# Kernel optimization log

Hardware: AMD Instinct MI355X
Metric: run time of the kernel (lower is better)

## Reference

```python
import jax, jax.numpy as jnp
import numpy as np

B, T, I, H, FC, O = 256, 4096, 63, 50, 64, 2


def setup_inputs() -> dict:
    key = jax.random.key(0)
    ks = jax.random.split(key, 9)
    s_ih = 1.0 / np.sqrt(H)
    inp = {
        "x": jax.random.normal(ks[0], (B, T, I), dtype=jnp.float32),
        # RNN params (PyTorch layout: W_ih [H, I], W_hh [H, H])
        "W_ih": jax.random.uniform(ks[1], (H, I), jnp.float32, -s_ih, s_ih),
        "b_ih": jax.random.uniform(ks[2], (H,), jnp.float32, -s_ih, s_ih),
        "W_hh": jax.random.uniform(ks[3], (H, H), jnp.float32, -s_ih, s_ih),
        "b_hh": jax.random.uniform(ks[4], (H,), jnp.float32, -s_ih, s_ih),
        # MLP head
        "W1": jax.random.uniform(ks[5], (FC, H), jnp.float32, -1.0 / np.sqrt(H), 1.0 / np.sqrt(H)),
        "b1": jax.random.uniform(ks[6], (FC,), jnp.float32, -1.0 / np.sqrt(H), 1.0 / np.sqrt(H)),
        "W2": jax.random.uniform(ks[7], (O, FC), jnp.float32, -1.0 / np.sqrt(FC), 1.0 / np.sqrt(FC)),
        "b2": jax.random.uniform(ks[8], (O,), jnp.float32, -1.0 / np.sqrt(FC), 1.0 / np.sqrt(FC)),
    }
    return inp


def reference(x, W_ih, b_ih, W_hh, b_hh, W1, b1, W2, b2):
    # Precompute input projection for all timesteps in one GEMM: [B, T, H]
    xz = jnp.einsum("bti,hi->bth", x, W_ih) + b_ih
    h0 = jnp.zeros((x.shape[0], W_hh.shape[0]), x.dtype)

    def step(h, xt):  # h: [B, H], xt: [B, H]
        h_new = jnp.tanh(xt + h @ W_hh.T + b_hh)
        return h_new, None

    # scan over time; only the final hidden state is needed (out[:, -1, :])
    hT, _ = jax.lax.scan(step, h0, jnp.swapaxes(xz, 0, 1))
    out = jax.nn.relu(hT @ W1.T + b1) @ W2.T + b2  # [B, O]
    probs = jax.nn.softmax(out, axis=1)
    return jnp.argmax(probs, axis=1).astype(jnp.float32)  # [B]
```

## Files before the change

### kernel.cpp

```cpp
#include <hip/hip_runtime.h>
#include <cstdint>
#include <cstddef>

#define BB 256
#define TT 4096
#define ID 63
#define HH 50
#define FCD 64

__device__ __forceinline__ float readlane_f(float v, int lane) {
    return __int_as_float(__builtin_amdgcn_readlane(__float_as_int(v), lane));
}

__device__ __forceinline__ float fast_tanh(float x) {
    float a = fabsf(x);
    float e = __builtin_amdgcn_exp2f(a * -2.88539008177792681472f);
    float r = (1.0f - e) * __builtin_amdgcn_rcpf(1.0f + e);
    return copysignf(r, x);
}

__global__ __launch_bounds__(64) void proj_kernel(
    const float* __restrict__ x, const float* __restrict__ W_ih,
    const float* __restrict__ b_ih, const float* __restrict__ b_hh,
    float* __restrict__ z)
{
    __shared__ float xs[64 * ID];
    const int lane = threadIdx.x;
    const int64_t row0 = (int64_t)blockIdx.x * 64;
    const float* __restrict__ xin = x + row0 * ID;

#pragma unroll
    for (int i = lane; i < 64 * ID; i += 64) xs[i] = xin[i];
    __syncthreads();

    float xr[ID];
#pragma unroll
    for (int i = 0; i < ID; ++i) xr[i] = xs[lane * ID + i];

    float* __restrict__ zout = z + (row0 + lane) * HH;
#pragma unroll 2
    for (int j = 0; j < HH; ++j) {
        float a0 = b_ih[j] + b_hh[j], a1 = 0.f, a2 = 0.f, a3 = 0.f;
#pragma unroll
        for (int i = 0; i < 60; i += 4) {
            a0 += xr[i + 0] * W_ih[j * ID + i + 0];
            a1 += xr[i + 1] * W_ih[j * ID + i + 1];
            a2 += xr[i + 2] * W_ih[j * ID + i + 2];
            a3 += xr[i + 3] * W_ih[j * ID + i + 3];
        }
        a0 += xr[60] * W_ih[j * ID + 60];
        a1 += xr[61] * W_ih[j * ID + 61];
        a2 += xr[62] * W_ih[j * ID + 62];
        zout[j] = (a0 + a2) + (a1 + a3);
    }
}

template <int FUSED>
__global__ __launch_bounds__(64) void rnn_kernel(
    const float* __restrict__ zx, const float* __restrict__ W_ih,
    const float* __restrict__ b_ih, const float* __restrict__ W_hh,
    const float* __restrict__ b_hh, const float* __restrict__ W1,
    const float* __restrict__ b1, const float* __restrict__ W2,
    const float* __restrict__ b2, float* __restrict__ out)
{
    const int b = blockIdx.x;
    const int lane = threadIdx.x;
    const int j = (lane < HH) ? lane : (HH - 1);

    float whh[HH];
#pragma unroll
    for (int k = 0; k < HH; ++k) whh[k] = W_hh[j * HH + k];

    float wih[FUSED ? ID : 1];
    float bias = 0.f;
    const float* __restrict__ base;
    int col, ld;
    if (FUSED) {
#pragma unroll
        for (int i = 0; i < ID; ++i) wih[i] = W_ih[j * ID + i];
        bias = b_ih[j] + b_hh[j];
        base = zx + (int64_t)b * TT * ID;
        ld = ID;
        col = (lane < ID) ? lane : (ID - 1);
    } else {
        base = zx + (int64_t)b * TT * HH;
        ld = HH;
        col = j;
    }

    float zp[8], zn[8];
#pragma unroll
    for (int u = 0; u < 8; ++u) zp[u] = base[u * ld + col];

    float vh = 0.f;
    for (int t0 = 0; t0 < TT; t0 += 8) {
#pragma unroll
        for (int u = 0; u < 8; ++u) {
            int tt = t0 + 8 + u;
            if (tt > TT - 1) tt = TT - 1;
            zn[u] = base[(int64_t)tt * ld + col];
        }
#pragma unroll
        for (int u = 0; u < 8; ++u) {
            float a0, a1, a2, a3;
            if (FUSED) {
                a0 = bias; a1 = 0.f; a2 = 0.f; a3 = 0.f;
#pragma unroll
                for (int i = 0; i < 60; i += 4) {
                    a0 += readlane_f(zp[u], i + 0) * wih[i + 0];
                    a1 += readlane_f(zp[u], i + 1) * wih[i + 1];
                    a2 += readlane_f(zp[u], i + 2) * wih[i + 2];
                    a3 += readlane_f(zp[u], i + 3) * wih[i + 3];
                }
                a0 += readlane_f(zp[u], 60) * wih[60];
                a1 += readlane_f(zp[u], 61) * wih[61];
                a2 += readlane_f(zp[u], 62) * wih[62];
            } else {
                a0 = zp[u]; a1 = 0.f; a2 = 0.f; a3 = 0.f;
            }
#pragma unroll
            for (int k = 0; k < 48; k += 4) {
                a0 += readlane_f(vh, k + 0) * whh[k + 0];
                a1 += readlane_f(vh, k + 1) * whh[k + 1];
                a2 += readlane_f(vh, k + 2) * whh[k + 2];
                a3 += readlane_f(vh, k + 3) * whh[k + 3];
            }
            a0 += readlane_f(vh, 48) * whh[48];
            a1 += readlane_f(vh, 49) * whh[49];
            vh = fast_tanh((a0 + a2) + (a1 + a3));
        }
#pragma unroll
        for (int u = 0; u < 8; ++u) zp[u] = zn[u];
    }

    float f = b1[lane];
#pragma unroll
    for (int k = 0; k < HH; ++k) f += readlane_f(vh, k) * W1[lane * HH + k];
    f = fmaxf(f, 0.f);
    float p0 = f * W2[lane];
    float p1 = f * W2[FCD + lane];
#pragma unroll
    for (int off = 32; off > 0; off >>= 1) {
        p0 += __shfl_down(p0, off, 64);
        p1 += __shfl_down(p1, off, 64);
    }
    if (lane == 0) out[b] = ((p1 + b2[1]) > (p0 + b2[0])) ? 1.0f : 0.0f;
}

extern "C" void kernel_launch(void* const* d_in, const int* in_sizes, int n_in,
                              void* d_out, int out_size, void* d_ws, size_t ws_size,
                              hipStream_t stream)
{
    const float* x    = (const float*)d_in[0];
    const float* W_ih = (const float*)d_in[1];
    const float* b_ih = (const float*)d_in[2];
    const float* W_hh = (const float*)d_in[3];
    const float* b_hh = (const float*)d_in[4];
    const float* W1   = (const float*)d_in[5];
    const float* b1   = (const float*)d_in[6];
    const float* W2   = (const float*)d_in[7];
    const float* b2   = (const float*)d_in[8];
    float* out = (float*)d_out;

    const size_t zbytes = (size_t)BB * TT * HH * sizeof(float);
    if (ws_size >= zbytes) {
        float* z = (float*)d_ws;
        proj_kernel<<<(BB * TT) / 64, 64, 0, stream>>>(x, W_ih, b_ih, b_hh, z);
        rnn_kernel<0><<<BB, 64, 0, stream>>>(z, W_ih, b_ih, W_hh, b_hh,
                                             W1, b1, W2, b2, out);
    } else {
        rnn_kernel<1><<<BB, 64, 0, stream>>>(x, W_ih, b_ih, W_hh, b_hh,
                                             W1, b1, W2, b2, out);
    }
}
```

Before: 1.464 ms.

## Use packed FP32 FMA for recurrence, vectorize projection IO, simplify tanh

The recurrent matvec now reads the hidden state into SGPR pairs with readlane and accumulates through v_pk_mul/v_pk_fma_f32 on packed weight pairs. This halves the VALU FMA count on the serial per-timestep critical path. The projection kernel loads x as float4, stages its outputs in shared memory and writes them out with coalesced float2 stores. tanh drops the abs/copysign steps, and prefetch clamping becomes a branch. The inline asm with 64-bit SGPR operands risks extra s_mov work, and the simplified tanh may lose accuracy or overflow to inf for large negative inputs.

```diff
diff --git a/kernel.cpp b/kernel.cpp
--- a/kernel.cpp
+++ b/kernel.cpp
@@ -8,15 +8,27 @@
 #define HH 50
 #define FCD 64
 
-__device__ __forceinline__ float readlane_f(float v, int lane) {
+typedef float f32x2 __attribute__((ext_vector_type(2)));
+
+__device__ __forceinline__ uint32_t rl_u32(float v, int lane) {
+    return (uint32_t)__builtin_amdgcn_readlane(__float_as_int(v), lane);
+}
+__device__ __forceinline__ float rl_f(float v, int lane) {
     return __int_as_float(__builtin_amdgcn_readlane(__float_as_int(v), lane));
 }
 
+__device__ __forceinline__ f32x2 pk_mul(uint64_t hp, f32x2 w) {
+    f32x2 d;
+    asm("v_pk_mul_f32 %0, %1, %2" : "=v"(d) : "s"(hp), "v"(w));
+    return d;
+}
+__device__ __forceinline__ void pk_fma(f32x2& acc, uint64_t hp, f32x2 w) {
+    asm("v_pk_fma_f32 %0, %1, %2, %0" : "+v"(acc) : "s"(hp), "v"(w));
+}
+
 __device__ __forceinline__ float fast_tanh(float x) {
-    float a = fabsf(x);
-    float e = __builtin_amdgcn_exp2f(a * -2.88539008177792681472f);
-    float r = (1.0f - e) * __builtin_amdgcn_rcpf(1.0f + e);
-    return copysignf(r, x);
+    float e = __builtin_amdgcn_exp2f(x * 2.88539008177792681472f);
+    return 1.0f - 2.0f * __builtin_amdgcn_rcpf(e + 1.0f);
 }
 
 __global__ __launch_bounds__(64) void proj_kernel(
@@ -27,37 +39,113 @@
     __shared__ float xs[64 * ID];
     const int lane = threadIdx.x;
     const int64_t row0 = (int64_t)blockIdx.x * 64;
-    const float* __restrict__ xin = x + row0 * ID;
-
-#pragma unroll
-    for (int i = lane; i < 64 * ID; i += 64) xs[i] = xin[i];
+
+    const float4* __restrict__ xin4 = (const float4*)(x + row0 * ID);
+    float4* xs4 = (float4*)xs;
+    for (int i = lane; i < (64 * ID) / 4; i += 64) xs4[i] = xin4[i];
     __syncthreads();
 
     float xr[ID];
 #pragma unroll
     for (int i = 0; i < ID; ++i) xr[i] = xs[lane * ID + i];
-
-    float* __restrict__ zout = z + (row0 + lane) * HH;
-#pragma unroll 2
+    __syncthreads();
+
+    float* zs = xs;
+#pragma unroll 1
     for (int j = 0; j < HH; ++j) {
+        const float* __restrict__ wp = W_ih + j * ID;
         float a0 = b_ih[j] + b_hh[j], a1 = 0.f, a2 = 0.f, a3 = 0.f;
 #pragma unroll
         for (int i = 0; i < 60; i += 4) {
-            a0 += xr[i + 0] * W_ih[j * ID + i + 0];
-            a1 += xr[i + 1] * W_ih[j * ID + i + 1];
-            a2 += xr[i + 2] * W_ih[j * ID + i + 2];
-            a3 += xr[i + 3] * W_ih[j * ID + i + 3];
-        }
-        a0 += xr[60] * W_ih[j * ID + 60];
-        a1 += xr[61] * W_ih[j * ID + 61];
-        a2 += xr[62] * W_ih[j * ID + 62];
-        zout[j] = (a0 + a2) + (a1 + a3);
-    }
-}
-
-template <int FUSED>
+            a0 = fmaf(xr[i + 0], wp[i + 0], a0);
+            a1 = fmaf(xr[i + 1], wp[i + 1], a1);
+            a2 = fmaf(xr[i + 2], wp[i + 2], a2);
+            a3 = fmaf(xr[i + 3], wp[i + 3], a3);
+        }
+        a0 = fmaf(xr[60], wp[60], a0);
+        a1 = fmaf(xr[61], wp[61], a1);
+        a2 = fmaf(xr[62], wp[62], a2);
+        zs[lane * HH + j] = (a0 + a2) + (a1 + a3);
+    }
+    __syncthreads();
+
+    const float2* zs2 = (const float2*)zs;
+    float2* __restrict__ zo2 = (float2*)(z + row0 * HH);
+#pragma unroll
+    for (int i = lane; i < (64 * HH) / 2; i += 64) zo2[i] = zs2[i];
+}
+
 __global__ __launch_bounds__(64) void rnn_kernel(
-    const float* __restrict__ zx, const float* __restrict__ W_ih,
+    const float* __restrict__ z, const float* __restrict__ W_hh,
+    const float* __restrict__ W1, const float* __restrict__ b1,
+    const float* __restrict__ W2, const float* __restrict__ b2,
+    float* __restrict__ out)
+{
+    const int b = blockIdx.x;
+    const int lane = threadIdx.x;
+    const int j = (lane < HH) ? lane : (HH - 1);
+
+    f32x2 wpk[25];
+#pragma unroll
+    for (int k = 0; k < 25; ++k) {
+        wpk[k].x = W_hh[j * HH + 2 * k];
+        wpk[k].y = W_hh[j * HH + 2 * k + 1];
+    }
+
+    const float* __restrict__ base = z + (int64_t)b * TT * HH;
+    const int col = j;
+
+    float zp[8], zn[8];
+#pragma unroll
+    for (int u = 0; u < 8; ++u) zp[u] = base[u * HH + col];
+    const float* p = base + 8 * HH;
+
+    float vh = 0.f;
+    for (int t0 = 0; t0 < TT; t0 += 8) {
+        if (t0 + 8 < TT) {
+#pragma unroll
+            for (int u = 0; u < 8; ++u) zn[u] = p[u * HH + col];
+        }
+        p += 8 * HH;
+#pragma unroll
+        for (int u = 0; u < 8; ++u) {
+            uint64_t hp[25];
+#pragma unroll
+            for (int k = 0; k < 25; ++k) {
+                uint32_t lo = rl_u32(vh, 2 * k);
+                uint32_t hi = rl_u32(vh, 2 * k + 1);
+                hp[k] = (uint64_t)lo | ((uint64_t)hi << 32);
+            }
+            f32x2 accA = pk_mul(hp[0], wpk[0]);
+            f32x2 accB = pk_mul(hp[1], wpk[1]);
+#pragma unroll
+            for (int k = 2; k < 25; k += 2) pk_fma(accA, hp[k], wpk[k]);
+#pragma unroll
+            for (int k = 3; k < 25; k += 2) pk_fma(accB, hp[k], wpk[k]);
+            f32x2 ab = accA + accB;
+            float s = zp[u] + (ab.x + ab.y);
+            vh = fast_tanh(s);
+        }
+#pragma unroll
+        for (int u = 0; u < 8; ++u) zp[u] = zn[u];
+    }
+
+    float f = b1[lane];
+#pragma unroll
+    for (int k = 0; k < HH; ++k) f = fmaf(rl_f(vh, k), W1[lane * HH + k], f);
+    f = fmaxf(f, 0.f);
+    float p0 = f * W2[lane];
+    float p1 = f * W2[FCD + lane];
+#pragma unroll
+    for (int off = 32; off > 0; off >>= 1) {
+        p0 += __shfl_down(p0, off, 64);
+        p1 += __shfl_down(p1, off, 64);
+    }
+    if (lane == 0) out[b] = ((p1 + b2[1]) > (p0 + b2[0])) ? 1.0f : 0.0f;
+}
+
+__global__ __launch_bounds__(64) void rnn_fused_kernel(
+    const float* __restrict__ x, const float* __restrict__ W_ih,
     const float* __restrict__ b_ih, const float* __restrict__ W_hh,
     const float* __restrict__ b_hh, const float* __restrict__ W1,
     const float* __restrict__ b1, const float* __restrict__ W2,
@@ -70,63 +158,46 @@
     float whh[HH];
 #pragma unroll
     for (int k = 0; k < HH; ++k) whh[k] = W_hh[j * HH + k];
-
-    float wih[FUSED ? ID : 1];
-    float bias = 0.f;
-    const float* __restrict__ base;
-    int col, ld;
-    if (FUSED) {
-#pragma unroll
-        for (int i = 0; i < ID; ++i) wih[i] = W_ih[j * ID + i];
-        bias = b_ih[j] + b_hh[j];
-        base = zx + (int64_t)b * TT * ID;
-        ld = ID;
-        col = (lane < ID) ? lane : (ID - 1);
-    } else {
-        base = zx + (int64_t)b * TT * HH;
-        ld = HH;
-        col = j;
-    }
+    float wih[ID];
+#pragma unroll
+    for (int i = 0; i < ID; ++i) wih[i] = W_ih[j * ID + i];
+    const float bias = b_ih[j] + b_hh[j];
+
+    const float* __restrict__ base = x + (int64_t)b * TT * ID;
+    const int col = (lane < ID) ? lane : (ID - 1);
 
     float zp[8], zn[8];
 #pragma unroll
-    for (int u = 0; u < 8; ++u) zp[u] = base[u * ld + col];
+    for (int u = 0; u < 8; ++u) zp[u] = base[u * ID + col];
 
     float vh = 0.f;
     for (int t0 = 0; t0 < TT; t0 += 8) {
+        if (t0 + 8 < TT) {
+#pragma unroll
+            for (int u = 0; u < 8; ++u) zn[u] = base[(int64_t)(t0 + 8 + u) * ID + col];
+        }
 #pragma unroll
         for (int u = 0; u < 8; ++u) {
-            int tt = t0 + 8 + u;
-            if (tt > TT - 1) tt = TT - 1;
-            zn[u] = base[(int64_t)tt * ld + col];
-        }
-#pragma unroll
-        for (int u = 0; u < 8; ++u) {
-            float a0, a1, a2, a3;
-            if (FUSED) {
-                a0 = bias; a1 = 0.f; a2 = 0.f; a3 = 0.f;
-#pragma unroll
-                for (int i = 0; i < 60; i += 4) {
-                    a0 += readlane_f(zp[u], i + 0) * wih[i + 0];
-                    a1 += readlane_f(zp[u], i + 1) * wih[i + 1];
-                    a2 += readlane_f(zp[u], i + 2) * wih[i + 2];
-                    a3 += readlane_f(zp[u], i + 3) * wih[i + 3];
-                }
-                a0 += readlane_f(zp[u], 60) * wih[60];
-                a1 += readlane_f(zp[u], 61) * wih[61];
-                a2 += readlane_f(zp[u], 62) * wih[62];
-            } else {
-                a0 = zp[u]; a1 = 0.f; a2 = 0.f; a3 = 0.f;
+            float a0 = bias, a1 = 0.f, a2 = 0.f, a3 = 0.f;
+#pragma unroll
+            for (int i = 0; i < 60; i += 4) {
+                a0 = fmaf(rl_f(zp[u], i + 0), wih[i + 0], a0);
+                a1 = fmaf(rl_f(zp[u], i + 1), wih[i + 1], a1);
+                a2 = fmaf(rl_f(zp[u], i + 2), wih[i + 2], a2);
+                a3 = fmaf(rl_f(zp[u], i + 3), wih[i + 3], a3);
             }
+            a0 = fmaf(rl_f(zp[u], 60), wih[60], a0);
+            a1 = fmaf(rl_f(zp[u], 61), wih[61], a1);
+            a2 = fmaf(rl_f(zp[u], 62), wih[62], a2);
 #pragma unroll
             for (int k = 0; k < 48; k += 4) {
-                a0 += readlane_f(vh, k + 0) * whh[k + 0];
-                a1 += readlane_f(vh, k + 1) * whh[k + 1];
-                a2 += readlane_f(vh, k + 2) * whh[k + 2];
-                a3 += readlane_f(vh, k + 3) * whh[k + 3];
+                a0 = fmaf(rl_f(vh, k + 0), whh[k + 0], a0);
+                a1 = fmaf(rl_f(vh, k + 1), whh[k + 1], a1);
+                a2 = fmaf(rl_f(vh, k + 2), whh[k + 2], a2);
+                a3 = fmaf(rl_f(vh, k + 3), whh[k + 3], a3);
             }
-            a0 += readlane_f(vh, 48) * whh[48];
-            a1 += readlane_f(vh, 49) * whh[49];
+            a0 = fmaf(rl_f(vh, 48), whh[48], a0);
+            a1 = fmaf(rl_f(vh, 49), whh[49], a1);
             vh = fast_tanh((a0 + a2) + (a1 + a3));
         }
 #pragma unroll
@@ -135,7 +206,7 @@
 
     float f = b1[lane];
 #pragma unroll
-    for (int k = 0; k < HH; ++k) f += readlane_f(vh, k) * W1[lane * HH + k];
+    for (int k = 0; k < HH; ++k) f = fmaf(rl_f(vh, k), W1[lane * HH + k], f);
     f = fmaxf(f, 0.f);
     float p0 = f * W2[lane];
     float p1 = f * W2[FCD + lane];
@@ -166,10 +237,9 @@
     if (ws_size >= zbytes) {
         float* z = (float*)d_ws;
         proj_kernel<<<(BB * TT) / 64, 64, 0, stream>>>(x, W_ih, b_ih, b_hh, z);
-        rnn_kernel<0><<<BB, 64, 0, stream>>>(z, W_ih, b_ih, W_hh, b_hh,
-                                             W1, b1, W2, b2, out);
+        rnn_kernel<<<BB, 64, 0, stream>>>(z, W_hh, W1, b1, W2, b2, out);
     } else {
-        rnn_kernel<1><<<BB, 64, 0, stream>>>(x, W_ih, b_ih, W_hh, b_hh,
-                                             W1, b1, W2, b2, out);
-    }
-}
+        rnn_fused_kernel<<<BB, 64, 0, stream>>>(x, W_ih, b_ih, W_hh, b_hh,
+                                                W1, b1, W2, b2, out);
+    }
+}
```

After: 1.359 ms. 7.2% less time.
